# Kernel optimization log

Measured on AMD Instinct MI355X. Metric: run time of the kernel, lower is better.

The kernel has to match this reference:

```python
import jax, jax.numpy as jnp
import numpy as np

B, S, D_MODEL, H = 4, 4096, 1024, 16
HD = D_MODEL // H  # head_dim = 64


def setup_inputs() -> dict:
    key = jax.random.key(0)
    kq, kk, kv, kw, kb = jax.random.split(key, 5)
    Q = jax.random.normal(kq, (B, S, D_MODEL), dtype=jnp.float32)
    K = jax.random.normal(kk, (B, S, D_MODEL), dtype=jnp.float32)
    V = jax.random.normal(kv, (B, S, D_MODEL), dtype=jnp.float32)
    # out_proj: nn.Linear(d_model, d_model)
    lim = 1.0 / np.sqrt(D_MODEL)
    W_out = jax.random.uniform(kw, (D_MODEL, D_MODEL), jnp.float32, -lim, lim)
    b_out = jax.random.uniform(kb, (D_MODEL,), jnp.float32, -lim, lim)
    return {"Q": Q, "K": K, "V": V, "W_out": W_out, "b_out": b_out}


def reference(Q, K, V, W_out, b_out):
    b, s, d = Q.shape
    # split heads: [B, H, S, HD]
    Qh = Q.reshape(b, s, H, HD).transpose(0, 2, 1, 3)
    Kh = K.reshape(b, s, H, HD).transpose(0, 2, 1, 3)
    Vh = V.reshape(b, s, H, HD).transpose(0, 2, 1, 3)
    # linear attention reorder: KV = K^T V -> [B, H, HD, HD]
    KV = jnp.einsum('bhsd,bhse->bhde', Kh, Vh)
    # z = Q @ KV -> [B, H, S, HD]
    z = jnp.einsum('bhsd,bhde->bhse', Qh, KV)
    # merge heads -> [B, S, D]
    z = z.transpose(0, 2, 1, 3).reshape(b, s, d)
    # out_proj (torch Linear: x @ W^T + b, here W_out stored [out,in])
    return z @ W_out.T + b_out
```

## Files before the change

kernel.cpp:

```cpp
#include <hip/hip_runtime.h>
#include <hip/hip_bf16.h>

#define B_ 4
#define S_ 4096
#define DM 1024
#define H_ 16
#define HD 64
#define BH (B_*H_)
#define SPLIT 16
#define CHUNK (S_/SPLIT)

typedef __attribute__((ext_vector_type(8))) __bf16 bf16x8;
typedef __attribute__((ext_vector_type(4))) float f32x4;

#define MFMA16(a,b,c) __builtin_amdgcn_mfma_f32_16x16x32_bf16((a),(b),(c),0,0,0)

__device__ __forceinline__ void gload_lds16(const void* g, void* l) {
  __builtin_amdgcn_global_load_lds(
      (const __attribute__((address_space(1))) void*)g,
      (__attribute__((address_space(3))) void*)l, 16, 0, 0);
}

__global__ __launch_bounds__(256)
void k1_kv_partial(const float* __restrict__ Kg,
                   const float* __restrict__ Vg,
                   float* __restrict__ partial) {
  constexpr int LDP = 264;
  __shared__ __align__(16) __bf16 Kt[64 * LDP];
  __shared__ __align__(16) __bf16 Vt[64 * LDP];
  const int bid = blockIdx.x;
  const int split = bid >> 6;
  const int bh = bid & (BH - 1);
  const int b = bh >> 4, h = bh & 15;
  const int s0 = split * CHUNK;
  const int t = threadIdx.x;
  const float* Kbase = Kg + ((size_t)b * S_ + s0) * DM + h * HD;
  const float* Vbase = Vg + ((size_t)b * S_ + s0) * DM + h * HD;
  const int c = t & 15, sr = t >> 4;
  const int d0 = c * 4;
#pragma unroll
  for (int it = 0; it < 16; ++it) {
    const int s = it * 16 + sr;
    f32x4 kv = *reinterpret_cast<const f32x4*>(Kbase + (size_t)s * DM + d0);
    f32x4 vv = *reinterpret_cast<const f32x4*>(Vbase + (size_t)s * DM + d0);
#pragma unroll
    for (int j = 0; j < 4; ++j) {
      Kt[(d0 + j) * LDP + s] = (__bf16)kv[j];
      Vt[(d0 + j) * LDP + s] = (__bf16)vv[j];
    }
  }
  __syncthreads();
  const int w = t >> 6, l = t & 63, lr = l & 15, lg = l >> 4;
  f32x4 acc[4] = {};
#pragma unroll
  for (int ks = 0; ks < 8; ++ks) {
    bf16x8 a = *reinterpret_cast<const bf16x8*>(&Kt[(w * 16 + lr) * LDP + ks * 32 + lg * 8]);
#pragma unroll
    for (int n = 0; n < 4; ++n) {
      bf16x8 bb = *reinterpret_cast<const bf16x8*>(&Vt[(n * 16 + lr) * LDP + ks * 32 + lg * 8]);
      acc[n] = MFMA16(a, bb, acc[n]);
    }
  }
  float* dst = partial + ((size_t)(split * BH + bh) << 12);
#pragma unroll
  for (int n = 0; n < 4; ++n)
#pragma unroll
    for (int r = 0; r < 4; ++r) {
      const int d = w * 16 + lg * 4 + r;
      const int e = n * 16 + lr;
      dst[d * 64 + e] = acc[n][r];
    }
}

__global__ __launch_bounds__(256)
void k2_kv_reduce(const float* __restrict__ partial,
                  __bf16* __restrict__ kvt) {
  const int bid = blockIdx.x;
  const int bh = bid >> 2, q = bid & 3;
  const int t = threadIdx.x;
#pragma unroll
  for (int i = 0; i < 4; ++i) {
    const int idx = q * 1024 + i * 256 + t;
    float s = 0.f;
#pragma unroll
    for (int sp = 0; sp < SPLIT; ++sp)
      s += partial[((size_t)(sp * BH + bh) << 12) + idx];
    kvt[((size_t)bh << 12) + idx] = (__bf16)s;
  }
}

__global__ __launch_bounds__(256)
void k25_u(const float* __restrict__ Wg,
           const __bf16* __restrict__ kvt,
           __bf16* __restrict__ Ut) {
  const int bid = blockIdx.x;
  const int bh = bid >> 2, nblk = bid & 3;
  const int b = bh >> 4, h = bh & 15;
  const int t = threadIdx.x, w = t >> 6, l = t & 63, lr = l & 15, lg = l >> 4;
  const int n0w = nblk * 256 + w * 64;
  const __bf16* kvb = kvt + ((size_t)bh << 12);
  f32x4 acc[4][4] = {};
#pragma unroll
  for (int ks = 0; ks < 2; ++ks) {
    bf16x8 bfr[4];
#pragma unroll
    for (int nf = 0; nf < 4; ++nf)
      bfr[nf] = *reinterpret_cast<const bf16x8*>(kvb + (nf * 16 + lr) * 64 + ks * 32 + lg * 8);
#pragma unroll
    for (int mf = 0; mf < 4; ++mf) {
      const int n = n0w + mf * 16 + lr;
      const float* wp = Wg + (size_t)n * DM + h * 64 + ks * 32 + lg * 8;
      f32x4 w0 = *reinterpret_cast<const f32x4*>(wp);
      f32x4 w1 = *reinterpret_cast<const f32x4*>(wp + 4);
      bf16x8 af;
#pragma unroll
      for (int j = 0; j < 4; ++j) { af[j] = (__bf16)w0[j]; af[4 + j] = (__bf16)w1[j]; }
#pragma unroll
      for (int nf = 0; nf < 4; ++nf)
        acc[mf][nf] = MFMA16(af, bfr[nf], acc[mf][nf]);
    }
  }
  __bf16* ub = Ut + ((size_t)b << 20);
#pragma unroll
  for (int mf = 0; mf < 4; ++mf)
#pragma unroll
    for (int nf = 0; nf < 4; ++nf)
#pragma unroll
      for (int r = 0; r < 4; ++r) {
        const int n = n0w + mf * 16 + lg * 4 + r;
        ub[(size_t)n * DM + h * 64 + nf * 16 + lr] = (__bf16)acc[mf][nf][r];
      }
}

__global__ __launch_bounds__(256)
void k4_out_gemm(const float* __restrict__ Qg,
                 const __bf16* __restrict__ Ut,
                 const float* __restrict__ biasg,
                 float* __restrict__ outg) {
  __shared__ __align__(16) __bf16 Alds[128 * 64];
  __shared__ __align__(16) __bf16 Blds[128 * 64];
  const int bid = blockIdx.x;
  const int b = bid >> 8, rem = bid & 255;
  const int nblk = rem >> 5, mblk = rem & 31;
  const int m0 = mblk * 128, n0 = nblk * 128;
  const int t = threadIdx.x, wid = t >> 6, l = t & 63, lr = l & 15, lg = l >> 4;
  const int wr = wid >> 1, wc = wid & 1;
  const float* Qb = Qg + (size_t)b * S_ * DM;
  const __bf16* Ub = Ut + ((size_t)b << 20);
  f32x4 acc[4][4] = {};

  const int srow = (t >> 3), sc = t & 7;
  bf16x8 aregs[4];

#pragma unroll
  for (int it = 0; it < 4; ++it) {
    const int row = it * 32 + srow;
    const float* qp = Qb + (size_t)(m0 + row) * DM + sc * 8;
    f32x4 lo = *reinterpret_cast<const f32x4*>(qp);
    f32x4 hi = *reinterpret_cast<const f32x4*>(qp + 4);
#pragma unroll
    for (int j = 0; j < 4; ++j) { aregs[it][j] = (__bf16)lo[j]; aregs[it][4 + j] = (__bf16)hi[j]; }
  }

  for (int kt = 0; kt < 16; ++kt) {
    const int k0 = kt * 64;
#pragma unroll
    for (int it = 0; it < 4; ++it) {
      const int row = it * 32 + srow;
      const int gc = sc ^ (row & 7);
      gload_lds16((const void*)(Ub + (size_t)(n0 + row) * DM + k0 + gc * 8),
                  (void*)((char*)Blds + (it * 256 + wid * 64) * 16));
    }
#pragma unroll
    for (int it = 0; it < 4; ++it) {
      const int row = it * 32 + srow;
      const int ch = sc ^ (row & 7);
      *reinterpret_cast<bf16x8*>((char*)Alds + row * 128 + ch * 16) = aregs[it];
    }
    __syncthreads();
    if (kt < 15) {
#pragma unroll
      for (int it = 0; it < 4; ++it) {
        const int row = it * 32 + srow;
        const float* qp = Qb + (size_t)(m0 + row) * DM + (k0 + 64) + sc * 8;
        f32x4 lo = *reinterpret_cast<const f32x4*>(qp);
        f32x4 hi = *reinterpret_cast<const f32x4*>(qp + 4);
#pragma unroll
        for (int j = 0; j < 4; ++j) { aregs[it][j] = (__bf16)lo[j]; aregs[it][4 + j] = (__bf16)hi[j]; }
      }
    }
#pragma unroll
    for (int ks = 0; ks < 2; ++ks) {
      bf16x8 af[4], bfr[4];
#pragma unroll
      for (int mt = 0; mt < 4; ++mt) {
        const int row = wr * 64 + mt * 16 + lr;
        const int ch = (ks * 4 + lg) ^ (row & 7);
        af[mt] = *reinterpret_cast<const bf16x8*>((const char*)Alds + row * 128 + ch * 16);
      }
#pragma unroll
      for (int nt = 0; nt < 4; ++nt) {
        const int row = wc * 64 + nt * 16 + lr;
        const int ch = (ks * 4 + lg) ^ (row & 7);
        bfr[nt] = *reinterpret_cast<const bf16x8*>((const char*)Blds + row * 128 + ch * 16);
      }
#pragma unroll
      for (int mt = 0; mt < 4; ++mt)
#pragma unroll
        for (int nt = 0; nt < 4; ++nt)
          acc[mt][nt] = MFMA16(af[mt], bfr[nt], acc[mt][nt]);
    }
    __syncthreads();
  }

#pragma unroll
  for (int nt = 0; nt < 4; ++nt) {
    const int colg = n0 + wc * 64 + nt * 16 + lr;
    const float bv = biasg[colg];
#pragma unroll
    for (int mt = 0; mt < 4; ++mt)
#pragma unroll
      for (int r = 0; r < 4; ++r) {
        const int rowg = m0 + wr * 64 + mt * 16 + lg * 4 + r;
        outg[((size_t)b * S_ + rowg) * DM + colg] = acc[mt][nt][r] + bv;
      }
  }
}

extern "C" void kernel_launch(void* const* d_in, const int* in_sizes, int n_in,
                              void* d_out, int out_size, void* d_ws, size_t ws_size,
                              hipStream_t stream) {
  const float* Q = (const float*)d_in[0];
  const float* K = (const float*)d_in[1];
  const float* V = (const float*)d_in[2];
  const float* W = (const float*)d_in[3];
  const float* bias = (const float*)d_in[4];
  float* out = (float*)d_out;

  char* ws = (char*)d_ws;
  float* partial = (float*)ws;
  __bf16* kvt = (__bf16*)(ws + 16777216);
  __bf16* Ut  = (__bf16*)(ws + 16777216 + 524288);

  hipLaunchKernelGGL(k1_kv_partial, dim3(SPLIT * BH), dim3(256), 0, stream, K, V, partial);
  hipLaunchKernelGGL(k2_kv_reduce, dim3(BH * 4), dim3(256), 0, stream, partial, kvt);
  hipLaunchKernelGGL(k25_u, dim3(BH * 4), dim3(256), 0, stream, W, kvt, Ut);
  hipLaunchKernelGGL(k4_out_gemm, dim3(1024), dim3(256), 0, stream, Q, Ut, bias, out);
}
```

Baseline: 134.3 us.

## Pre-convert Q to bf16 in KV kernel and async-load it in output GEMM

The first kernel now also reads Q and writes a bf16 copy to workspace, alongside its existing K/V streaming. The output GEMM then loads both A (Q) and B (U) tiles straight into LDS with global_load_lds. This replaces the register-staged fp32 load and convert, which each of the 8 column blocks repeated per Q tile. In exchange it adds a 32MB bf16 write and read-back, and it needs a larger workspace.

Result: faster. 121.3 us (-9.7%).

```diff
diff --git a/kernel.cpp b/kernel.cpp
--- a/kernel.cpp
+++ b/kernel.cpp
@@ -11,6 +11,7 @@
 #define CHUNK (S_/SPLIT)
 
 typedef __attribute__((ext_vector_type(8))) __bf16 bf16x8;
+typedef __attribute__((ext_vector_type(4))) __bf16 bf16x4;
 typedef __attribute__((ext_vector_type(4))) float f32x4;
 
 #define MFMA16(a,b,c) __builtin_amdgcn_mfma_f32_16x16x32_bf16((a),(b),(c),0,0,0)
@@ -22,9 +23,11 @@
 }
 
 __global__ __launch_bounds__(256)
-void k1_kv_partial(const float* __restrict__ Kg,
+void k1_kv_partial(const float* __restrict__ Qg,
+                   const float* __restrict__ Kg,
                    const float* __restrict__ Vg,
-                   float* __restrict__ partial) {
+                   float* __restrict__ partial,
+                   __bf16* __restrict__ Qb) {
   constexpr int LDP = 264;
   __shared__ __align__(16) __bf16 Kt[64 * LDP];
   __shared__ __align__(16) __bf16 Vt[64 * LDP];
@@ -34,8 +37,11 @@
   const int b = bh >> 4, h = bh & 15;
   const int s0 = split * CHUNK;
   const int t = threadIdx.x;
-  const float* Kbase = Kg + ((size_t)b * S_ + s0) * DM + h * HD;
-  const float* Vbase = Vg + ((size_t)b * S_ + s0) * DM + h * HD;
+  const size_t base = ((size_t)b * S_ + s0) * DM + h * HD;
+  const float* Kbase = Kg + base;
+  const float* Vbase = Vg + base;
+  const float* Qbase = Qg + base;
+  __bf16* Qbb = Qb + base;
   const int c = t & 15, sr = t >> 4;
   const int d0 = c * 4;
 #pragma unroll
@@ -43,11 +49,15 @@
     const int s = it * 16 + sr;
     f32x4 kv = *reinterpret_cast<const f32x4*>(Kbase + (size_t)s * DM + d0);
     f32x4 vv = *reinterpret_cast<const f32x4*>(Vbase + (size_t)s * DM + d0);
+    f32x4 qv = *reinterpret_cast<const f32x4*>(Qbase + (size_t)s * DM + d0);
+    bf16x4 qo;
 #pragma unroll
     for (int j = 0; j < 4; ++j) {
       Kt[(d0 + j) * LDP + s] = (__bf16)kv[j];
       Vt[(d0 + j) * LDP + s] = (__bf16)vv[j];
-    }
+      qo[j] = (__bf16)qv[j];
+    }
+    *reinterpret_cast<bf16x4*>(Qbb + (size_t)s * DM + d0) = qo;
   }
   __syncthreads();
   const int w = t >> 6, l = t & 63, lr = l & 15, lg = l >> 4;
@@ -133,7 +143,7 @@
 }
 
 __global__ __launch_bounds__(256)
-void k4_out_gemm(const float* __restrict__ Qg,
+void k4_out_gemm(const __bf16* __restrict__ Qb,
                  const __bf16* __restrict__ Ut,
                  const float* __restrict__ biasg,
                  float* __restrict__ outg) {
@@ -145,50 +155,23 @@
   const int m0 = mblk * 128, n0 = nblk * 128;
   const int t = threadIdx.x, wid = t >> 6, l = t & 63, lr = l & 15, lg = l >> 4;
   const int wr = wid >> 1, wc = wid & 1;
-  const float* Qb = Qg + (size_t)b * S_ * DM;
-  const __bf16* Ub = Ut + ((size_t)b << 20);
+  const __bf16* Ab = Qb + (size_t)b * S_ * DM;
+  const __bf16* Bb = Ut + ((size_t)b << 20);
   f32x4 acc[4][4] = {};
-
-  const int srow = (t >> 3), sc = t & 7;
-  bf16x8 aregs[4];
-
-#pragma unroll
-  for (int it = 0; it < 4; ++it) {
-    const int row = it * 32 + srow;
-    const float* qp = Qb + (size_t)(m0 + row) * DM + sc * 8;
-    f32x4 lo = *reinterpret_cast<const f32x4*>(qp);
-    f32x4 hi = *reinterpret_cast<const f32x4*>(qp + 4);
-#pragma unroll
-    for (int j = 0; j < 4; ++j) { aregs[it][j] = (__bf16)lo[j]; aregs[it][4 + j] = (__bf16)hi[j]; }
-  }
 
   for (int kt = 0; kt < 16; ++kt) {
     const int k0 = kt * 64;
 #pragma unroll
     for (int it = 0; it < 4; ++it) {
-      const int row = it * 32 + srow;
-      const int gc = sc ^ (row & 7);
-      gload_lds16((const void*)(Ub + (size_t)(n0 + row) * DM + k0 + gc * 8),
+      const int idx = it * 256 + t;
+      const int row = idx >> 3, c = idx & 7;
+      const int gc = c ^ (row & 7);
+      gload_lds16((const void*)(Ab + (size_t)(m0 + row) * DM + k0 + gc * 8),
+                  (void*)((char*)Alds + (it * 256 + wid * 64) * 16));
+      gload_lds16((const void*)(Bb + (size_t)(n0 + row) * DM + k0 + gc * 8),
                   (void*)((char*)Blds + (it * 256 + wid * 64) * 16));
     }
-#pragma unroll
-    for (int it = 0; it < 4; ++it) {
-      const int row = it * 32 + srow;
-      const int ch = sc ^ (row & 7);
-      *reinterpret_cast<bf16x8*>((char*)Alds + row * 128 + ch * 16) = aregs[it];
-    }
     __syncthreads();
-    if (kt < 15) {
-#pragma unroll
-      for (int it = 0; it < 4; ++it) {
-        const int row = it * 32 + srow;
-        const float* qp = Qb + (size_t)(m0 + row) * DM + (k0 + 64) + sc * 8;
-        f32x4 lo = *reinterpret_cast<const f32x4*>(qp);
-        f32x4 hi = *reinterpret_cast<const f32x4*>(qp + 4);
-#pragma unroll
-        for (int j = 0; j < 4; ++j) { aregs[it][j] = (__bf16)lo[j]; aregs[it][4 + j] = (__bf16)hi[j]; }
-      }
-    }
 #pragma unroll
     for (int ks = 0; ks < 2; ++ks) {
       bf16x8 af[4], bfr[4];
@@ -239,11 +222,12 @@
 
   char* ws = (char*)d_ws;
   float* partial = (float*)ws;
-  __bf16* kvt = (__bf16*)(ws + 16777216);
-  __bf16* Ut  = (__bf16*)(ws + 16777216 + 524288);
-
-  hipLaunchKernelGGL(k1_kv_partial, dim3(SPLIT * BH), dim3(256), 0, stream, K, V, partial);
+  __bf16* kvt = (__bf16*)(ws + (16u << 20));
+  __bf16* Ut  = (__bf16*)(ws + (16u << 20) + (512u << 10));
+  __bf16* Qb  = (__bf16*)(ws + (25u << 20));
+
+  hipLaunchKernelGGL(k1_kv_partial, dim3(SPLIT * BH), dim3(256), 0, stream, Q, K, V, partial, Qb);
   hipLaunchKernelGGL(k2_kv_reduce, dim3(BH * 4), dim3(256), 0, stream, partial, kvt);
   hipLaunchKernelGGL(k25_u, dim3(BH * 4), dim3(256), 0, stream, W, kvt, Ut);
-  hipLaunchKernelGGL(k4_out_gemm, dim3(1024), dim3(256), 0, stream, Q, Ut, bias, out);
-}
+  hipLaunchKernelGGL(k4_out_gemm, dim3(1024), dim3(256), 0, stream, Qb, Ut, bias, out);
+}
```
